# Optimization experiments

Hardware: AMD Instinct MI355X
Metric: run time of the kernel (lower is better)

Reference implementation:

```python
import jax, jax.numpy as jnp
import numpy as np

B, M, H, D, C = 512, 40, 128, 64, 128


def setup_inputs() -> dict:
    key = jax.random.key(0)
    k1, k2, k3, k4 = jax.random.split(key, 4)
    x0 = jax.random.normal(k1, (B, M, D), dtype=jnp.float32)
    xk = jax.random.normal(k2, (B, H, D), dtype=jnp.float32)
    # Conv1d(kernel_size=1) weight [C, H*M, 1] squeezed to [C, H*M]; bias [C]
    W = jax.random.normal(k3, (C, H * M), dtype=jnp.float32) * 0.02
    b = jax.random.normal(k4, (C,), dtype=jnp.float32) * 0.02
    return {"x0": x0, "xk": xk, "W": W, "b": b}


def reference(x0, xk, W, b):
    # torch: outer[b, h*M+m, d] = xk[b,h,d] * x0[b,m,d]; out = conv1d(outer)
    # conv1d with kernel_size=1 is a channel contraction:
    #   out[b,c,d] = sum_{h,m} W[c, h*M+m] * xk[b,h,d] * x0[b,m,d] + b[c]
    Bsz, Hh, Dd = xk.shape
    Mm = x0.shape[1]
    Cc = W.shape[0]
    Wr = W.reshape(Cc, Hh, Mm)  # channel index is h*M + m -> [C, H, M]
    out = jnp.einsum('bhd,bmd,chm->bcd', xk, x0, Wr) + b[None, :, None]
    return out  # [B, C, D]
```

## Files before the change

kernel.cpp:

```cpp
#include <hip/hip_runtime.h>
#include <hip/hip_bf16.h>

typedef __attribute__((ext_vector_type(8))) short short8;
typedef __attribute__((ext_vector_type(4))) float f32x4;
typedef unsigned short u16;
typedef unsigned int u32;

#define NB 512
#define NM 40
#define NH 128
#define ND 64
#define NC 128
#define KTOT 5120

__device__ __forceinline__ u16 f2bf_rne(float f) {
    u32 u = __float_as_uint(f);
    u32 r = u + 0x7FFFu + ((u >> 16) & 1u);
    return (u16)(r >> 16);
}

__device__ __forceinline__ void gload16(const void* g, void* l) {
    __builtin_amdgcn_global_load_lds(
        (const __attribute__((address_space(1))) void*)g,
        (__attribute__((address_space(3))) void*)l, 16, 0, 0);
}

__global__ void w3_kernel(const float* __restrict__ W, u16* __restrict__ W3) {
    __shared__ u16 kbuf[NH * 20];
    const int c = blockIdx.x >> 1, mh = blockIdx.x & 1;
    const float* src = W + (size_t)c * KTOT + mh * 20;
    for (int i = threadIdx.x; i < NH * 5; i += 256) {
        int h = i / 5, j4 = i % 5;
        float4 v = *(const float4*)(src + h * NM + j4 * 4);
        u16* kb = kbuf + h * 20 + j4 * 4;
        kb[0] = f2bf_rne(v.x); kb[1] = f2bf_rne(v.y);
        kb[2] = f2bf_rne(v.z); kb[3] = f2bf_rne(v.w);
    }
    __syncthreads();
    for (int i = threadIdx.x; i < 320; i += 256) {
        int mo = i >> 4, t = (i >> 2) & 3, q = i & 3;
        int n = (mh * 20 + mo) * 16 + t * 4 + q;
        union { short8 s8; u16 e[8]; } v;
#pragma unroll
        for (int j = 0; j < 8; ++j)
            v.e[j] = kbuf[(t * 32 + q * 8 + j) * 20 + mo];
        *(short8*)(W3 + ((size_t)n * 128 + c) * 8) = v.s8;
    }
}

__global__ void __launch_bounds__(512, 4) cin_main(
    const float* __restrict__ x0g, const float* __restrict__ xkg,
    const float* __restrict__ biasg, const u16* __restrict__ W3,
    float* __restrict__ out)
{
    __shared__ __align__(16) char smem[62592];
    char*  ring   = smem;
    float* red    = (float*)smem;
    short* xkT    = (short*)(smem + 32768);
    float* x0s    = (float*)(smem + 51200);
    float* bias_s = (float*)(smem + 62080);

    const int tid = threadIdx.x;
    const int w = tid >> 6, L = tid & 63;
    const int q = L >> 4, l16 = L & 15;
    const int kh = w & 1;
    const int rh = w >> 1;
    const int ch = blockIdx.x & 1;
    const size_t b = blockIdx.x >> 1;

    const char* A0 = (const char*)W3
        + (size_t)(kh * 16384 + q * 2048 + (ch * 64 + rh * 16 + l16) * 16);
    char* ringw = ring + w * 4096;

    auto stage = [&](int ua, int slot) {
        gload16(A0 + (size_t)(ua >> 1) * 32768 + (size_t)(ua & 1) * 8192,
                ringw + slot * 1024 + L * 16);
    };
    stage(0, 0); stage(1, 1); stage(2, 2);

    for (int i = tid; i < 2048; i += 512) {
        int h = i >> 4, d4 = (i & 15) << 2;
        float4 v = *(const float4*)(xkg + b * (NH * ND) + h * ND + d4);
        xkT[(d4 + 0) * 144 + h] = (short)f2bf_rne(v.x);
        xkT[(d4 + 1) * 144 + h] = (short)f2bf_rne(v.y);
        xkT[(d4 + 2) * 144 + h] = (short)f2bf_rne(v.z);
        xkT[(d4 + 3) * 144 + h] = (short)f2bf_rne(v.w);
    }
    for (int i = tid; i < 640; i += 512) {
        int m = i >> 4, d4 = (i & 15) << 2;
        *(f32x4*)(x0s + m * 68 + d4) =
            *(const f32x4*)(x0g + b * (NM * ND) + m * ND + d4);
    }
    if (tid < NC) bias_s[tid] = biasg[tid];
    __syncthreads();

    const short* Bp = xkT + (size_t)l16 * 144 + kh * 64 + q * 8;
    short8 bR[2][4];
#pragma unroll
    for (int th = 0; th < 2; ++th)
#pragma unroll
        for (int n = 0; n < 4; ++n)
            bR[th][n] = *(const short8*)(Bp + n * (16 * 144) + th * 32);

    float s[4], sn[4];
#pragma unroll
    for (int n = 0; n < 4; ++n)
        s[n] = x0s[n * 16 + l16];

    f32x4 T[4] = {{0.f,0.f,0.f,0.f},{0.f,0.f,0.f,0.f},{0.f,0.f,0.f,0.f},{0.f,0.f,0.f,0.f}};
    f32x4 o[4] = {{0.f,0.f,0.f,0.f},{0.f,0.f,0.f,0.f},{0.f,0.f,0.f,0.f},{0.f,0.f,0.f,0.f}};

#pragma unroll 4
    for (int u = 0; u < 80; ++u) {
        const int th = u & 1;
        const int un = u + 3;
        stage((un < 80) ? un : 79, un & 3);
        asm volatile("s_waitcnt vmcnt(3)" ::: "memory");
        const short8 a = *(const short8*)(ringw + (u & 3) * 1024 + L * 16);
        if (th == 0) {
            const int m = u >> 1;
#pragma unroll
            for (int n = 0; n < 4; ++n)
                sn[n] = (m < 39) ? x0s[(m + 1) * 68 + n * 16 + l16] : 0.f;
        }
        T[0] = __builtin_amdgcn_mfma_f32_16x16x32_bf16(a, bR[th][0], T[0], 0, 0, 0);
        T[1] = __builtin_amdgcn_mfma_f32_16x16x32_bf16(a, bR[th][1], T[1], 0, 0, 0);
        T[2] = __builtin_amdgcn_mfma_f32_16x16x32_bf16(a, bR[th][2], T[2], 0, 0, 0);
        T[3] = __builtin_amdgcn_mfma_f32_16x16x32_bf16(a, bR[th][3], T[3], 0, 0, 0);
        if (th == 1) {
#pragma unroll
            for (int n = 0; n < 4; ++n) {
                const float dd = s[n] - sn[n];
                o[n] += dd * T[n];
                s[n] = sn[n];
            }
        }
    }

    asm volatile("s_waitcnt vmcnt(0)" ::: "memory");
    __syncthreads();

    float* myred = red + rh * 1280;
    if (kh == 1) {
#pragma unroll
        for (int n = 0; n < 4; ++n) {
            int d = n * 16 + l16;
            *(f32x4*)(myred + d * 20 + q * 4) = o[n];
        }
    }
    __syncthreads();
    if (kh == 0) {
        float* op = out + b * (NC * ND);
#pragma unroll
        for (int n = 0; n < 4; ++n) {
            int d = n * 16 + l16;
            f32x4 r = *(const f32x4*)(myred + d * 20 + q * 4);
#pragma unroll
            for (int rr = 0; rr < 4; ++rr) {
                int c = ch * 64 + rh * 16 + q * 4 + rr;
                op[c * ND + d] = o[n][rr] + r[rr] + bias_s[c];
            }
        }
    }
}

extern "C" void kernel_launch(void* const* d_in, const int* in_sizes, int n_in,
                              void* d_out, int out_size, void* d_ws, size_t ws_size,
                              hipStream_t stream) {
    const float* x0 = (const float*)d_in[0];
    const float* xk = (const float*)d_in[1];
    const float* W  = (const float*)d_in[2];
    const float* bi = (const float*)d_in[3];
    float* out = (float*)d_out;

    u16* W3 = (u16*)d_ws;

    w3_kernel<<<NC * 2, 256, 0, stream>>>(W, W3);
    cin_main<<<NB * 2, 512, 0, stream>>>(x0, xk, bi, W3, out);
}
```

Before: 126.2 us.

## Process two batches per block and load W tiles directly into registers

Each block now handles two batch elements and a quarter of the output channels with 256 threads. Every W3 A-fragment is reused across both batches' xk operands, so the MFMA work per weight load doubles. The LDS ring fed by global_load_lds is replaced by a two-deep register prefetch of A straight from global memory. The x0 differences (x0[m]-x0[m+1]) are precomputed into LDS before the loop, which drops the running s/sn bookkeeping. The cost is a larger register footprint and fewer, larger blocks, with launch bounds changed to 256 threads and 3 blocks per CU.

```diff
diff --git a/kernel.cpp b/kernel.cpp
--- a/kernel.cpp
+++ b/kernel.cpp
@@ -17,12 +17,6 @@
     u32 u = __float_as_uint(f);
     u32 r = u + 0x7FFFu + ((u >> 16) & 1u);
     return (u16)(r >> 16);
-}
-
-__device__ __forceinline__ void gload16(const void* g, void* l) {
-    __builtin_amdgcn_global_load_lds(
-        (const __attribute__((address_space(1))) void*)g,
-        (__attribute__((address_space(3))) void*)l, 16, 0, 0);
 }
 
 __global__ void w3_kernel(const float* __restrict__ W, u16* __restrict__ W3) {
@@ -48,117 +42,128 @@
     }
 }
 
-__global__ void __launch_bounds__(512, 4) cin_main(
+__global__ void __launch_bounds__(256, 3) cin_main(
     const float* __restrict__ x0g, const float* __restrict__ xkg,
     const float* __restrict__ biasg, const u16* __restrict__ W3,
     float* __restrict__ out)
 {
-    __shared__ __align__(16) char smem[62592];
-    char*  ring   = smem;
-    float* red    = (float*)smem;
-    short* xkT    = (short*)(smem + 32768);
-    float* x0s    = (float*)(smem + 51200);
-    float* bias_s = (float*)(smem + 62080);
+    __shared__ __align__(16) char smem[35328];
+    short* xkT    = (short*)smem;
+    float* x0d    = (float*)smem;
+    float* bias_s = (float*)(smem + 34816);
 
     const int tid = threadIdx.x;
     const int w = tid >> 6, L = tid & 63;
     const int q = L >> 4, l16 = L & 15;
     const int kh = w & 1;
     const int rh = w >> 1;
-    const int ch = blockIdx.x & 1;
-    const size_t b = blockIdx.x >> 1;
+    const int cq = blockIdx.x & 3;
+    const size_t b0 = 2 * (size_t)(blockIdx.x >> 2);
 
     const char* A0 = (const char*)W3
-        + (size_t)(kh * 16384 + q * 2048 + (ch * 64 + rh * 16 + l16) * 16);
-    char* ringw = ring + w * 4096;
+        + (size_t)(kh * 16384 + q * 2048 + (cq * 32 + rh * 16 + l16) * 16);
 
-    auto stage = [&](int ua, int slot) {
-        gload16(A0 + (size_t)(ua >> 1) * 32768 + (size_t)(ua & 1) * 8192,
-                ringw + slot * 1024 + L * 16);
-    };
-    stage(0, 0); stage(1, 1); stage(2, 2);
+    short8 aP[2];
+    aP[0] = *(const short8*)(A0);
+    aP[1] = *(const short8*)(A0 + 8192);
 
-    for (int i = tid; i < 2048; i += 512) {
-        int h = i >> 4, d4 = (i & 15) << 2;
-        float4 v = *(const float4*)(xkg + b * (NH * ND) + h * ND + d4);
-        xkT[(d4 + 0) * 144 + h] = (short)f2bf_rne(v.x);
-        xkT[(d4 + 1) * 144 + h] = (short)f2bf_rne(v.y);
-        xkT[(d4 + 2) * 144 + h] = (short)f2bf_rne(v.z);
-        xkT[(d4 + 3) * 144 + h] = (short)f2bf_rne(v.w);
-    }
-    for (int i = tid; i < 640; i += 512) {
-        int m = i >> 4, d4 = (i & 15) << 2;
-        *(f32x4*)(x0s + m * 68 + d4) =
-            *(const f32x4*)(x0g + b * (NM * ND) + m * ND + d4);
+    for (int i = tid; i < 4096; i += 256) {
+        int b2 = i >> 11, rem = i & 2047;
+        int h = rem >> 4, d4 = (rem & 15) << 2;
+        float4 v = *(const float4*)(xkg + (b0 + b2) * (NH * ND) + h * ND + d4);
+        short* xT = xkT + b2 * 8704;
+        xT[(d4 + 0) * 136 + h] = (short)f2bf_rne(v.x);
+        xT[(d4 + 1) * 136 + h] = (short)f2bf_rne(v.y);
+        xT[(d4 + 2) * 136 + h] = (short)f2bf_rne(v.z);
+        xT[(d4 + 3) * 136 + h] = (short)f2bf_rne(v.w);
     }
     if (tid < NC) bias_s[tid] = biasg[tid];
     __syncthreads();
 
-    const short* Bp = xkT + (size_t)l16 * 144 + kh * 64 + q * 8;
-    short8 bR[2][4];
+    short8 bR[2][2][4];
 #pragma unroll
-    for (int th = 0; th < 2; ++th)
+    for (int b2 = 0; b2 < 2; ++b2) {
+        const short* Bp = xkT + b2 * 8704 + (size_t)l16 * 136 + kh * 64 + q * 8;
 #pragma unroll
-        for (int n = 0; n < 4; ++n)
-            bR[th][n] = *(const short8*)(Bp + n * (16 * 144) + th * 32);
+        for (int th = 0; th < 2; ++th)
+#pragma unroll
+            for (int n = 0; n < 4; ++n)
+                bR[b2][th][n] = *(const short8*)(Bp + n * (16 * 136) + th * 32);
+    }
+    __syncthreads();
 
-    float s[4], sn[4];
-#pragma unroll
-    for (int n = 0; n < 4; ++n)
-        s[n] = x0s[n * 16 + l16];
+    for (int i = tid; i < 1280; i += 256) {
+        int b2 = i / 640, rem = i % 640;
+        int m = rem >> 4, d4 = (rem & 15) << 2;
+        const float* xp = x0g + (b0 + b2) * (NM * ND) + m * ND + d4;
+        float4 cur = *(const float4*)xp;
+        float4 nxt = make_float4(0.f, 0.f, 0.f, 0.f);
+        if (m < 39) nxt = *(const float4*)(xp + ND);
+        f32x4 dv;
+        dv[0] = cur.x - nxt.x; dv[1] = cur.y - nxt.y;
+        dv[2] = cur.z - nxt.z; dv[3] = cur.w - nxt.w;
+        *(f32x4*)(x0d + b2 * 2720 + m * 68 + d4) = dv;
+    }
+    __syncthreads();
 
-    f32x4 T[4] = {{0.f,0.f,0.f,0.f},{0.f,0.f,0.f,0.f},{0.f,0.f,0.f,0.f},{0.f,0.f,0.f,0.f}};
-    f32x4 o[4] = {{0.f,0.f,0.f,0.f},{0.f,0.f,0.f,0.f},{0.f,0.f,0.f,0.f},{0.f,0.f,0.f,0.f}};
+    const float* dd0 = x0d + (size_t)l16;
+
+    f32x4 T[2][4] = {};
+    f32x4 o[2][4] = {};
 
 #pragma unroll 4
     for (int u = 0; u < 80; ++u) {
         const int th = u & 1;
-        const int un = u + 3;
-        stage((un < 80) ? un : 79, un & 3);
-        asm volatile("s_waitcnt vmcnt(3)" ::: "memory");
-        const short8 a = *(const short8*)(ringw + (u & 3) * 1024 + L * 16);
-        if (th == 0) {
+        const short8 a = aP[u & 1];
+        const int up = (u + 2 < 80) ? (u + 2) : 79;
+        aP[u & 1] = *(const short8*)(A0 + (size_t)(up >> 1) * 32768
+                                        + (size_t)(up & 1) * 8192);
+        T[0][0] = __builtin_amdgcn_mfma_f32_16x16x32_bf16(a, bR[0][th][0], T[0][0], 0, 0, 0);
+        T[0][1] = __builtin_amdgcn_mfma_f32_16x16x32_bf16(a, bR[0][th][1], T[0][1], 0, 0, 0);
+        T[0][2] = __builtin_amdgcn_mfma_f32_16x16x32_bf16(a, bR[0][th][2], T[0][2], 0, 0, 0);
+        T[0][3] = __builtin_amdgcn_mfma_f32_16x16x32_bf16(a, bR[0][th][3], T[0][3], 0, 0, 0);
+        T[1][0] = __builtin_amdgcn_mfma_f32_16x16x32_bf16(a, bR[1][th][0], T[1][0], 0, 0, 0);
+        T[1][1] = __builtin_amdgcn_mfma_f32_16x16x32_bf16(a, bR[1][th][1], T[1][1], 0, 0, 0);
+        T[1][2] = __builtin_amdgcn_mfma_f32_16x16x32_bf16(a, bR[1][th][2], T[1][2], 0, 0, 0);
+        T[1][3] = __builtin_amdgcn_mfma_f32_16x16x32_bf16(a, bR[1][th][3], T[1][3], 0, 0, 0);
+        if (th == 1) {
             const int m = u >> 1;
 #pragma unroll
-            for (int n = 0; n < 4; ++n)
-                sn[n] = (m < 39) ? x0s[(m + 1) * 68 + n * 16 + l16] : 0.f;
-        }
-        T[0] = __builtin_amdgcn_mfma_f32_16x16x32_bf16(a, bR[th][0], T[0], 0, 0, 0);
-        T[1] = __builtin_amdgcn_mfma_f32_16x16x32_bf16(a, bR[th][1], T[1], 0, 0, 0);
-        T[2] = __builtin_amdgcn_mfma_f32_16x16x32_bf16(a, bR[th][2], T[2], 0, 0, 0);
-        T[3] = __builtin_amdgcn_mfma_f32_16x16x32_bf16(a, bR[th][3], T[3], 0, 0, 0);
-        if (th == 1) {
+            for (int b2 = 0; b2 < 2; ++b2)
 #pragma unroll
-            for (int n = 0; n < 4; ++n) {
-                const float dd = s[n] - sn[n];
-                o[n] += dd * T[n];
-                s[n] = sn[n];
-            }
+                for (int n = 0; n < 4; ++n) {
+                    const float dd = dd0[b2 * 2720 + m * 68 + n * 16];
+                    o[b2][n] += dd * T[b2][n];
+                }
         }
     }
 
-    asm volatile("s_waitcnt vmcnt(0)" ::: "memory");
     __syncthreads();
-
-    float* myred = red + rh * 1280;
+    float* red = (float*)smem;
+    float* myred = red + (rh * 2) * 1280;
     if (kh == 1) {
 #pragma unroll
-        for (int n = 0; n < 4; ++n) {
-            int d = n * 16 + l16;
-            *(f32x4*)(myred + d * 20 + q * 4) = o[n];
-        }
+        for (int b2 = 0; b2 < 2; ++b2)
+#pragma unroll
+            for (int n = 0; n < 4; ++n) {
+                int d = n * 16 + l16;
+                *(f32x4*)(myred + b2 * 1280 + d * 20 + q * 4) = o[b2][n];
+            }
     }
     __syncthreads();
     if (kh == 0) {
-        float* op = out + b * (NC * ND);
 #pragma unroll
-        for (int n = 0; n < 4; ++n) {
-            int d = n * 16 + l16;
-            f32x4 r = *(const f32x4*)(myred + d * 20 + q * 4);
+        for (int b2 = 0; b2 < 2; ++b2) {
+            float* op = out + (b0 + b2) * (NC * ND);
 #pragma unroll
-            for (int rr = 0; rr < 4; ++rr) {
-                int c = ch * 64 + rh * 16 + q * 4 + rr;
-                op[c * ND + d] = o[n][rr] + r[rr] + bias_s[c];
+            for (int n = 0; n < 4; ++n) {
+                int d = n * 16 + l16;
+                f32x4 r = *(const f32x4*)(myred + b2 * 1280 + d * 20 + q * 4);
+#pragma unroll
+                for (int rr = 0; rr < 4; ++rr) {
+                    int c = cq * 32 + rh * 16 + q * 4 + rr;
+                    op[c * ND + d] = o[b2][n][rr] + r[rr] + bias_s[c];
+                }
             }
         }
     }
@@ -176,5 +181,5 @@
     u16* W3 = (u16*)d_ws;
 
     w3_kernel<<<NC * 2, 256, 0, stream>>>(W, W3);
-    cin_main<<<NB * 2, 512, 0, stream>>>(x0, xk, bi, W3, out);
+    cin_main<<<NB / 2 * 4, 256, 0, stream>>>(x0, xk, bi, W3, out);
 }
```

After: 130.8 us. 3.7% more time.
